# Kernel optimization log

Hardware: AMD Instinct MI355X
Metric: run time of the kernel (lower is better)

Reference implementation:

```python
import jax, jax.numpy as jnp
import numpy as np

B, NMAX, H, C, HID = 256, 512, 256, 64, 512
NEG = jnp.float32(-1e9)

def setup_inputs() -> dict:
    key = jax.random.key(0)
    ks = jax.random.split(key, 12)
    s_in = 1.0 / np.sqrt(2 * H + C)
    s_h = 1.0 / np.sqrt(HID)
    return {
        "nodes_hv": jax.random.normal(ks[0], (B, NMAX, H), jnp.float32),
        "class_cond": jax.random.normal(ks[1], (B, C), jnp.float32),
        "W1": jax.random.normal(ks[2], (2 * H + C, HID), jnp.float32) * s_in,
        "b1": jnp.zeros((HID,), jnp.float32),
        "W2": jax.random.normal(ks[3], (HID, HID), jnp.float32) * s_h,
        "b2": jnp.zeros((HID,), jnp.float32),
        "W3": jax.random.normal(ks[4], (HID, 1), jnp.float32) * s_h,
        "b3": jnp.zeros((1,), jnp.float32),
        "dirns": jax.random.randint(ks[5], (B,), 0, 2, jnp.int32),
        "node_counts": jax.random.randint(ks[6], (B,), NMAX // 2 + 1, NMAX, jnp.int32),
        "dests": jax.random.randint(ks[7], (B,), 0, NMAX // 2, jnp.int32),
    }

def reference(nodes_hv, class_cond, W1, b1, W2, b2, W3, b3, dirns, node_counts, dests):
    Bb, Nmax, Hh = nodes_hv.shape
    D = Nmax - 1  # padded number of candidate destinations
    # per-graph newest node embedding: hv[b, n_b - 1]
    src_idx = (node_counts - 1).astype(jnp.int32)
    src_embed = jnp.take_along_axis(nodes_hv, src_idx[:, None, None], axis=1)  # [B,1,H]
    src_b = jnp.broadcast_to(src_embed, (Bb, D, Hh))
    cand = nodes_hv[:, :D, :]  # candidate (old-node) embeddings, padded
    # dirn == 1: edge new->old, so (src_side, dest_side) = (cand, new); else (new, cand)
    dirn1 = (dirns == 1)[:, None, None]
    side_a = jnp.where(dirn1, cand, src_b)
    side_b = jnp.where(dirn1, src_b, cand)
    cc = jnp.broadcast_to(class_cond[:, None, :], (Bb, D, class_cond.shape[-1]))
    x = jnp.concatenate([side_a, side_b, cc], axis=2)  # [B, D, 2H+C]
    h = jax.nn.relu(jnp.einsum("bdi,ih->bdh", x, W1) + b1)
    h = jax.nn.relu(jnp.einsum("bdi,ih->bdh", h, W2) + b2)
    scores = (jnp.einsum("bdi,io->bdo", h, W3) + b3)[..., 0]  # [B, D]
    # ragged validity: graph b has n_b - 1 candidates
    valid = jnp.arange(D)[None, :] < (node_counts - 1)[:, None]
    scores = jnp.where(valid, scores, NEG)
    logp = jax.nn.log_softmax(scores, axis=1)
    loss = -jnp.take_along_axis(logp, dests[:, None].astype(jnp.int32), axis=1)[:, 0]  # [B]
    return loss
```

## Files before the change

kernel.cpp:

```cpp
#include <hip/hip_runtime.h>
#include <math.h>

#define BB    256
#define NMAX  512
#define HH    256
#define CC    64
#define HID   512
#define NEGV  -1000000000.0f
#define MT    32
#define SA_LD 264
#define SH_LD 520
#define TILE  512
#define KSTR  (32 * TILE)

typedef __attribute__((ext_vector_type(8))) short short8;
typedef __attribute__((ext_vector_type(4))) float floatx4;

__device__ inline ushort f2bf(float x) {
    unsigned u = __float_as_uint(x);
    u = (u + 0x7FFFu + ((u >> 16) & 1u)) >> 16;
    return (ushort)u;
}

__global__ __launch_bounds__(256) void convert_swz(const float* __restrict__ W,
                                                   ushort* __restrict__ out) {
    const int kb = blockIdx.x, ntg = blockIdx.y;
    const int t = threadIdx.x;
    __shared__ float s[32][68];

    {
        const int kl = t >> 3, nn = (t & 7) * 8;
        const float* src = W + (size_t)(kb * 32 + kl) * HID + ntg * 64 + nn;
        *(float4*)&s[kl][nn]     = *(const float4*)src;
        *(float4*)&s[kl][nn + 4] = *(const float4*)(src + 4);
    }
    __syncthreads();

    const int ntl = t >> 6, ls = t & 63;
    const int qs = ls >> 4, l15s = ls & 15;
    short8 o;
    #pragma unroll
    for (int j = 0; j < 8; ++j)
        o[j] = (short)f2bf(s[qs * 8 + j][ntl * 16 + l15s]);
    const int nt = ntg * 4 + ntl;
    *(short8*)(out + ((size_t)(kb * 32 + nt)) * TILE + ls * 8) = o;
}

__global__ __launch_bounds__(256) void base_kernel(
    const float* __restrict__ nodes_hv, const float* __restrict__ class_cond,
    const float* __restrict__ W1, const float* __restrict__ b1,
    const int* __restrict__ dirns, const int* __restrict__ node_counts,
    float* __restrict__ v_ws)
{
    const int b = blockIdx.x;
    const int t = threadIdx.x;
    __shared__ float s_src[HH];
    __shared__ float s_cc[CC];

    const int nc   = node_counts[b];
    const int dirn = dirns[b];
    const int src_idx = nc - 1;

    s_src[t] = nodes_hv[((size_t)b * NMAX + src_idx) * HH + t];
    if (t < CC) s_cc[t] = class_cond[b * CC + t];
    __syncthreads();

    const int srcoff = (dirn == 1) ? HH : 0;

    const int j = 2 * t;
    float acc0 = b1[j];
    float acc1 = b1[j + 1];

    #pragma unroll 4
    for (int r = 0; r < HH; ++r) {
        const float s = s_src[r];
        const float* wp = W1 + (size_t)(srcoff + r) * HID + j;
        acc0 += s * wp[0];
        acc1 += s * wp[1];
    }
    #pragma unroll 4
    for (int c = 0; c < CC; ++c) {
        const float s = s_cc[c];
        const float* wp = W1 + (size_t)(2 * HH + c) * HID + j;
        acc0 += s * wp[0];
        acc1 += s * wp[1];
    }
    v_ws[b * HID + j]     = acc0;
    v_ws[b * HID + j + 1] = acc1;
}

__global__ __launch_bounds__(256, 3) void mlp2(
    const float* __restrict__ nodes_hv,
    const ushort* __restrict__ Wt1s, const ushort* __restrict__ Wt2s,
    const float* __restrict__ b2, const float* __restrict__ W3,
    const float* __restrict__ b3,
    const int* __restrict__ dirns, const int* __restrict__ node_counts,
    const float* __restrict__ v_ws, float* __restrict__ scores)
{
    const int b  = blockIdx.y;
    const int d0 = blockIdx.x * MT;
    const int t  = threadIdx.x;
    const int lane = t & 63, wv = t >> 6;
    const int l15 = lane & 15, q = lane >> 4;

    __shared__ ushort s_a[MT * SA_LD];
    __shared__ ushort s_h[MT * SH_LD];
    __shared__ float  s_red[4][MT];

    const int nc = node_counts[b];
    const int kb0 = (dirns[b] == 1) ? 0 : 8;

    {
        const float4* src4 = (const float4*)nodes_hv + ((size_t)b * NMAX + d0) * (HH / 4);
        #pragma unroll
        for (int i = 0; i < (MT * HH / 4) / 256; ++i) {
            int idx = t + i * 256;
            int row = idx >> 6, c4 = idx & 63;
            float4 v = src4[idx];
            ushort4 p;
            p.x = f2bf(v.x); p.y = f2bf(v.y); p.z = f2bf(v.z); p.w = f2bf(v.w);
            *(ushort4*)&s_a[row * SA_LD + c4 * 4] = p;
        }
    }
    __syncthreads();

    floatx4 acc[2][8];
    #pragma unroll
    for (int mb = 0; mb < 2; ++mb)
        #pragma unroll
        for (int tn = 0; tn < 8; ++tn)
            acc[mb][tn] = (floatx4){0.f, 0.f, 0.f, 0.f};

    {
        const ushort* wb1 = Wt1s + ((size_t)kb0 * 32 + wv * 8) * TILE + lane * 8;
        #pragma unroll
        for (int ks = 0; ks < 8; ++ks) {
            const ushort* wp = wb1 + (size_t)ks * KSTR;
            short8 bfr[8];
            #pragma unroll
            for (int tn = 0; tn < 8; ++tn)
                bfr[tn] = *(const short8*)(wp + tn * TILE);
            short8 a0 = *(const short8*)&s_a[l15 * SA_LD + ks * 32 + q * 8];
            short8 a1 = *(const short8*)&s_a[(16 + l15) * SA_LD + ks * 32 + q * 8];
            #pragma unroll
            for (int tn = 0; tn < 8; ++tn) {
                acc[0][tn] = __builtin_amdgcn_mfma_f32_16x16x32_bf16(a0, bfr[tn], acc[0][tn], 0, 0, 0);
                acc[1][tn] = __builtin_amdgcn_mfma_f32_16x16x32_bf16(a1, bfr[tn], acc[1][tn], 0, 0, 0);
            }
        }
    }

    const int n0 = wv * 128;

    #pragma unroll
    for (int tn = 0; tn < 8; ++tn) {
        const int n = n0 + tn * 16 + l15;
        const float v = v_ws[b * HID + n];
        #pragma unroll
        for (int mb = 0; mb < 2; ++mb)
            #pragma unroll
            for (int r = 0; r < 4; ++r) {
                float h = acc[mb][tn][r] + v;
                h = h > 0.f ? h : 0.f;
                s_h[(mb * 16 + q * 4 + r) * SH_LD + n] = f2bf(h);
            }
    }
    __syncthreads();

    #pragma unroll
    for (int mb = 0; mb < 2; ++mb)
        #pragma unroll
        for (int tn = 0; tn < 8; ++tn)
            acc[mb][tn] = (floatx4){0.f, 0.f, 0.f, 0.f};
    {
        const ushort* wb2 = Wt2s + ((size_t)wv * 8) * TILE + lane * 8;
        #pragma unroll
        for (int ks = 0; ks < 16; ++ks) {
            const ushort* wp = wb2 + (size_t)ks * KSTR;
            short8 bfr[8];
            #pragma unroll
            for (int tn = 0; tn < 8; ++tn)
                bfr[tn] = *(const short8*)(wp + tn * TILE);
            short8 a0 = *(const short8*)&s_h[l15 * SH_LD + ks * 32 + q * 8];
            short8 a1 = *(const short8*)&s_h[(16 + l15) * SH_LD + ks * 32 + q * 8];
            #pragma unroll
            for (int tn = 0; tn < 8; ++tn) {
                acc[0][tn] = __builtin_amdgcn_mfma_f32_16x16x32_bf16(a0, bfr[tn], acc[0][tn], 0, 0, 0);
                acc[1][tn] = __builtin_amdgcn_mfma_f32_16x16x32_bf16(a1, bfr[tn], acc[1][tn], 0, 0, 0);
            }
        }
    }

    float p[2][4] = {{0.f, 0.f, 0.f, 0.f}, {0.f, 0.f, 0.f, 0.f}};
    #pragma unroll
    for (int tn = 0; tn < 8; ++tn) {
        const int n  = n0 + tn * 16 + l15;
        const float bb = b2[n];
        const float w3 = W3[n];
        #pragma unroll
        for (int mb = 0; mb < 2; ++mb)
            #pragma unroll
            for (int r = 0; r < 4; ++r) {
                float h = acc[mb][tn][r] + bb;
                h = h > 0.f ? h : 0.f;
                p[mb][r] += h * w3;
            }
    }
    #pragma unroll
    for (int mb = 0; mb < 2; ++mb)
        #pragma unroll
        for (int r = 0; r < 4; ++r) {
            float v = p[mb][r];
            v += __shfl_xor(v, 1, 64);
            v += __shfl_xor(v, 2, 64);
            v += __shfl_xor(v, 4, 64);
            v += __shfl_xor(v, 8, 64);
            if (l15 == 0) s_red[wv][mb * 16 + q * 4 + r] = v;
        }
    __syncthreads();
    if (t < MT) {
        const float s = s_red[0][t] + s_red[1][t] + s_red[2][t] + s_red[3][t] + b3[0];
        const int d = d0 + t;
        scores[b * NMAX + d] = (d < nc - 1) ? s : NEGV;
    }
}

__global__ __launch_bounds__(256) void loss_kernel(
    const float* __restrict__ scores, const int* __restrict__ dests,
    float* __restrict__ out)
{
    const int b = blockIdx.x;
    const int t = threadIdx.x;
    __shared__ float red[4];

    const float s0 = scores[b * NMAX + t];
    const float s1 = scores[b * NMAX + t + 256];

    const int lane = t & 63, wv = t >> 6;

    float mx = fmaxf(s0, s1);
    #pragma unroll
    for (int off = 32; off > 0; off >>= 1) mx = fmaxf(mx, __shfl_down(mx, off, 64));
    if (lane == 0) red[wv] = mx;
    __syncthreads();
    mx = fmaxf(fmaxf(red[0], red[1]), fmaxf(red[2], red[3]));
    __syncthreads();

    float e = __expf(s0 - mx) + __expf(s1 - mx);
    #pragma unroll
    for (int off = 32; off > 0; off >>= 1) e += __shfl_down(e, off, 64);
    if (lane == 0) red[wv] = e;
    __syncthreads();

    if (t == 0) {
        const float sum = red[0] + red[1] + red[2] + red[3];
        const float sd = scores[b * NMAX + dests[b]];
        out[b] = -(sd - mx - logf(sum));
    }
}

extern "C" void kernel_launch(void* const* d_in, const int* in_sizes, int n_in,
                              void* d_out, int out_size, void* d_ws, size_t ws_size,
                              hipStream_t stream) {
    const float* nodes_hv    = (const float*)d_in[0];
    const float* class_cond  = (const float*)d_in[1];
    const float* W1          = (const float*)d_in[2];
    const float* b1          = (const float*)d_in[3];
    const float* W2          = (const float*)d_in[4];
    const float* b2          = (const float*)d_in[5];
    const float* W3          = (const float*)d_in[6];
    const float* b3          = (const float*)d_in[7];
    const int*   dirns       = (const int*)d_in[8];
    const int*   node_counts = (const int*)d_in[9];
    const int*   dests       = (const int*)d_in[10];
    float* out = (float*)d_out;

    ushort* Wt1s   = (ushort*)d_ws;
    ushort* Wt2s   = Wt1s + 16 * KSTR;
    float*  v_ws   = (float*)(Wt2s + 16 * KSTR);
    float*  scores = v_ws + BB * HID;

    convert_swz<<<dim3(16, 8), 256, 0, stream>>>(W1, Wt1s);
    convert_swz<<<dim3(16, 8), 256, 0, stream>>>(W2, Wt2s);
    base_kernel<<<BB, 256, 0, stream>>>(nodes_hv, class_cond, W1, b1,
                                        dirns, node_counts, v_ws);
    mlp2<<<dim3(NMAX / MT, BB), 256, 0, stream>>>(
        nodes_hv, Wt1s, Wt2s, b2, W3, b3, dirns, node_counts, v_ws, scores);
    loss_kernel<<<BB, 256, 0, stream>>>(scores, dests, out);
}
```

Measured before the change: 355.8 us.

## Merge prep kernels into one launch and alias LDS buffers for higher occupancy

Folds the two weight-conversion launches and the per-graph base-vector launch into a single prep kernel, with each block choosing its task by index, which removes two kernel launches. In the main MLP kernel the input tile and hidden tile now share one LDS buffer, with an extra barrier before the hidden tile overwrites it. Launch bounds rise from 3 to 4 blocks per CU so more blocks can be resident. The trade-offs are one added synchronization and a tighter register budget, which could cause spills.

```diff
diff --git a/kernel.cpp b/kernel.cpp
--- a/kernel.cpp
+++ b/kernel.cpp
@@ -22,74 +22,79 @@
     return (ushort)u;
 }
 
-__global__ __launch_bounds__(256) void convert_swz(const float* __restrict__ W,
-                                                   ushort* __restrict__ out) {
-    const int kb = blockIdx.x, ntg = blockIdx.y;
-    const int t = threadIdx.x;
-    __shared__ float s[32][68];
-
-    {
-        const int kl = t >> 3, nn = (t & 7) * 8;
-        const float* src = W + (size_t)(kb * 32 + kl) * HID + ntg * 64 + nn;
-        *(float4*)&s[kl][nn]     = *(const float4*)src;
-        *(float4*)&s[kl][nn + 4] = *(const float4*)(src + 4);
-    }
-    __syncthreads();
-
-    const int ntl = t >> 6, ls = t & 63;
-    const int qs = ls >> 4, l15s = ls & 15;
-    short8 o;
-    #pragma unroll
-    for (int j = 0; j < 8; ++j)
-        o[j] = (short)f2bf(s[qs * 8 + j][ntl * 16 + l15s]);
-    const int nt = ntg * 4 + ntl;
-    *(short8*)(out + ((size_t)(kb * 32 + nt)) * TILE + ls * 8) = o;
-}
-
-__global__ __launch_bounds__(256) void base_kernel(
+__global__ __launch_bounds__(256) void prep_kernel(
+    const float* __restrict__ W1, const float* __restrict__ W2,
+    ushort* __restrict__ Wt1s, ushort* __restrict__ Wt2s,
     const float* __restrict__ nodes_hv, const float* __restrict__ class_cond,
-    const float* __restrict__ W1, const float* __restrict__ b1,
+    const float* __restrict__ b1,
     const int* __restrict__ dirns, const int* __restrict__ node_counts,
     float* __restrict__ v_ws)
 {
-    const int b = blockIdx.x;
+    const int blk = blockIdx.x;
     const int t = threadIdx.x;
+
+    __shared__ float s_conv[32][68];
     __shared__ float s_src[HH];
     __shared__ float s_cc[CC];
 
-    const int nc   = node_counts[b];
-    const int dirn = dirns[b];
-    const int src_idx = nc - 1;
-
-    s_src[t] = nodes_hv[((size_t)b * NMAX + src_idx) * HH + t];
-    if (t < CC) s_cc[t] = class_cond[b * CC + t];
-    __syncthreads();
-
-    const int srcoff = (dirn == 1) ? HH : 0;
-
-    const int j = 2 * t;
-    float acc0 = b1[j];
-    float acc1 = b1[j + 1];
-
-    #pragma unroll 4
-    for (int r = 0; r < HH; ++r) {
-        const float s = s_src[r];
-        const float* wp = W1 + (size_t)(srcoff + r) * HID + j;
-        acc0 += s * wp[0];
-        acc1 += s * wp[1];
-    }
-    #pragma unroll 4
-    for (int c = 0; c < CC; ++c) {
-        const float s = s_cc[c];
-        const float* wp = W1 + (size_t)(2 * HH + c) * HID + j;
-        acc0 += s * wp[0];
-        acc1 += s * wp[1];
-    }
-    v_ws[b * HID + j]     = acc0;
-    v_ws[b * HID + j + 1] = acc1;
-}
-
-__global__ __launch_bounds__(256, 3) void mlp2(
+    if (blk < 256) {
+        const float* W = (blk < 128) ? W1 : W2;
+        ushort* out    = (blk < 128) ? Wt1s : Wt2s;
+        const int bb  = blk & 127;
+        const int kb  = bb >> 3, ntg = bb & 7;
+
+        {
+            const int kl = t >> 3, nn = (t & 7) * 8;
+            const float* src = W + (size_t)(kb * 32 + kl) * HID + ntg * 64 + nn;
+            *(float4*)&s_conv[kl][nn]     = *(const float4*)src;
+            *(float4*)&s_conv[kl][nn + 4] = *(const float4*)(src + 4);
+        }
+        __syncthreads();
+
+        const int ntl = t >> 6, ls = t & 63;
+        const int qs = ls >> 4, l15s = ls & 15;
+        short8 o;
+        #pragma unroll
+        for (int j = 0; j < 8; ++j)
+            o[j] = (short)f2bf(s_conv[qs * 8 + j][ntl * 16 + l15s]);
+        const int nt = ntg * 4 + ntl;
+        *(short8*)(out + ((size_t)(kb * 32 + nt)) * TILE + ls * 8) = o;
+    } else {
+        const int b = blk - 256;
+        const int nc   = node_counts[b];
+        const int dirn = dirns[b];
+        const int src_idx = nc - 1;
+
+        s_src[t] = nodes_hv[((size_t)b * NMAX + src_idx) * HH + t];
+        if (t < CC) s_cc[t] = class_cond[b * CC + t];
+        __syncthreads();
+
+        const int srcoff = (dirn == 1) ? HH : 0;
+
+        const int j = 2 * t;
+        float acc0 = b1[j];
+        float acc1 = b1[j + 1];
+
+        #pragma unroll 4
+        for (int r = 0; r < HH; ++r) {
+            const float s = s_src[r];
+            const float* wp = W1 + (size_t)(srcoff + r) * HID + j;
+            acc0 += s * wp[0];
+            acc1 += s * wp[1];
+        }
+        #pragma unroll 4
+        for (int c = 0; c < CC; ++c) {
+            const float s = s_cc[c];
+            const float* wp = W1 + (size_t)(2 * HH + c) * HID + j;
+            acc0 += s * wp[0];
+            acc1 += s * wp[1];
+        }
+        v_ws[b * HID + j]     = acc0;
+        v_ws[b * HID + j + 1] = acc1;
+    }
+}
+
+__global__ __launch_bounds__(256, 4) void mlp2(
     const float* __restrict__ nodes_hv,
     const ushort* __restrict__ Wt1s, const ushort* __restrict__ Wt2s,
     const float* __restrict__ b2, const float* __restrict__ W3,
@@ -103,8 +108,7 @@
     const int lane = t & 63, wv = t >> 6;
     const int l15 = lane & 15, q = lane >> 4;
 
-    __shared__ ushort s_a[MT * SA_LD];
-    __shared__ ushort s_h[MT * SH_LD];
+    __shared__ ushort s_u[MT * SH_LD];
     __shared__ float  s_red[4][MT];
 
     const int nc = node_counts[b];
@@ -119,7 +123,7 @@
             float4 v = src4[idx];
             ushort4 p;
             p.x = f2bf(v.x); p.y = f2bf(v.y); p.z = f2bf(v.z); p.w = f2bf(v.w);
-            *(ushort4*)&s_a[row * SA_LD + c4 * 4] = p;
+            *(ushort4*)&s_u[row * SA_LD + c4 * 4] = p;
         }
     }
     __syncthreads();
@@ -140,8 +144,8 @@
             #pragma unroll
             for (int tn = 0; tn < 8; ++tn)
                 bfr[tn] = *(const short8*)(wp + tn * TILE);
-            short8 a0 = *(const short8*)&s_a[l15 * SA_LD + ks * 32 + q * 8];
-            short8 a1 = *(const short8*)&s_a[(16 + l15) * SA_LD + ks * 32 + q * 8];
+            short8 a0 = *(const short8*)&s_u[l15 * SA_LD + ks * 32 + q * 8];
+            short8 a1 = *(const short8*)&s_u[(16 + l15) * SA_LD + ks * 32 + q * 8];
             #pragma unroll
             for (int tn = 0; tn < 8; ++tn) {
                 acc[0][tn] = __builtin_amdgcn_mfma_f32_16x16x32_bf16(a0, bfr[tn], acc[0][tn], 0, 0, 0);
@@ -149,6 +153,7 @@
             }
         }
     }
+    __syncthreads();
 
     const int n0 = wv * 128;
 
@@ -162,7 +167,7 @@
             for (int r = 0; r < 4; ++r) {
                 float h = acc[mb][tn][r] + v;
                 h = h > 0.f ? h : 0.f;
-                s_h[(mb * 16 + q * 4 + r) * SH_LD + n] = f2bf(h);
+                s_u[(mb * 16 + q * 4 + r) * SH_LD + n] = f2bf(h);
             }
     }
     __syncthreads();
@@ -181,8 +186,8 @@
             #pragma unroll
             for (int tn = 0; tn < 8; ++tn)
                 bfr[tn] = *(const short8*)(wp + tn * TILE);
-            short8 a0 = *(const short8*)&s_h[l15 * SH_LD + ks * 32 + q * 8];
-            short8 a1 = *(const short8*)&s_h[(16 + l15) * SH_LD + ks * 32 + q * 8];
+            short8 a0 = *(const short8*)&s_u[l15 * SH_LD + ks * 32 + q * 8];
+            short8 a1 = *(const short8*)&s_u[(16 + l15) * SH_LD + ks * 32 + q * 8];
             #pragma unroll
             for (int tn = 0; tn < 8; ++tn) {
                 acc[0][tn] = __builtin_amdgcn_mfma_f32_16x16x32_bf16(a0, bfr[tn], acc[0][tn], 0, 0, 0);
@@ -280,10 +285,9 @@
     float*  v_ws   = (float*)(Wt2s + 16 * KSTR);
     float*  scores = v_ws + BB * HID;
 
-    convert_swz<<<dim3(16, 8), 256, 0, stream>>>(W1, Wt1s);
-    convert_swz<<<dim3(16, 8), 256, 0, stream>>>(W2, Wt2s);
-    base_kernel<<<BB, 256, 0, stream>>>(nodes_hv, class_cond, W1, b1,
-                                        dirns, node_counts, v_ws);
+    prep_kernel<<<512, 256, 0, stream>>>(W1, W2, Wt1s, Wt2s,
+                                         nodes_hv, class_cond, b1,
+                                         dirns, node_counts, v_ws);
     mlp2<<<dim3(NMAX / MT, BB), 256, 0, stream>>>(
         nodes_hv, Wt1s, Wt2s, b2, W3, b3, dirns, node_counts, v_ws, scores);
     loss_kernel<<<BB, 256, 0, stream>>>(scores, dests, out);
```

Result: no change. 352.6 us (-0.9%).
